# Performance work log

Hardware: AMD Instinct MI355X
Metric: run time of the kernel (lower is better)

## Reference

```python
import jax, jax.numpy as jnp
import numpy as np

B, S, N, T, F, E = 8, 4, 2000, 16, 10, 16
R = 8                      # rnn_hidden_unit
H1, H2 = 2 * R, R          # per-stock hidden sizes of lstm1 / lstm2
NH, DK, DV = 4, 8, 8       # attention heads / dims
DM = H2 * N                # attention model dim
D = R * T                  # node feature dim for hypergraph conv
MLP = 16
SLOPE = 0.1

def _layernorm(x, g, b, eps=1e-5):
    mu = x.mean(-1, keepdims=True)
    var = ((x - mu) ** 2).mean(-1, keepdims=True)
    return (x - mu) * jax.lax.rsqrt(var + eps) * g + b

def _lstm(x, W, U, b, h):
    # x: [B, N, T, e]; shared per-stock LSTM, scanned over time
    xt = jnp.moveaxis(x, 2, 0)                      # [T, B, N, e]
    z0 = jnp.zeros((x.shape[0], x.shape[1], h), x.dtype)
    def step(carry, xi):
        hp, cp = carry
        z = xi @ W + hp @ U + b                     # [B, N, 4h]
        i, f, g_, o = jnp.split(z, 4, axis=-1)
        c = jax.nn.sigmoid(f) * cp + jax.nn.sigmoid(i) * jnp.tanh(g_)
        hn = jax.nn.sigmoid(o) * jnp.tanh(c)
        return (hn, c), hn
    _, ys = jax.lax.scan(step, (z0, z0), xt)
    return jnp.moveaxis(ys, 0, 2)                   # [B, N, T, h]

def setup_inputs():
    key = jax.random.key(0)
    ks = jax.random.split(key, 24)
    g = lambda i, shape, s: jax.random.normal(ks[i], shape, dtype=jnp.float32) * s
    return {
        "inputs": jax.random.normal(ks[0], (B, N, T, F), dtype=jnp.float32),
        "emb_W": g(1, (F, E), 0.1), "emb_b": jnp.zeros((E,), jnp.float32),
        "W1": g(2, (E, 4 * H1), 0.1), "U1": g(3, (H1, 4 * H1), 0.1),
        "b1": jnp.zeros((4 * H1,), jnp.float32),
        "ln1_g": jnp.ones((N * H1,), jnp.float32), "ln1_b": jnp.zeros((N * H1,), jnp.float32),
        "W2": g(4, (H1, 4 * H2), 0.1), "U2": g(5, (H2, 4 * H2), 0.1),
        "b2": jnp.zeros((4 * H2,), jnp.float32),
        "Wq": g(6, (DM, NH * DK), 0.02), "Wk": g(7, (DM, NH * DK), 0.02),
        "Wv": g(8, (DM, NH * DV), 0.02), "Wo": g(9, (NH * DV, DM), 0.02),
        "ln2_g": jnp.ones((DM,), jnp.float32), "ln2_b": jnp.zeros((DM,), jnp.float32),
        "par": jax.random.uniform(ks[10], (S,), jnp.float32, 0.0, 0.99),
        "theta1": g(11, (D, D), 0.05), "diag1": jnp.ones((N,), jnp.float32),
        "theta2": g(12, (D, D), 0.05), "diag2": jnp.ones((N,), jnp.float32),
        "mlp1_W": g(13, (2 * R, MLP), 0.2), "mlp1_b": jnp.zeros((MLP,), jnp.float32),
        "mlp2_W": g(14, (MLP, 1), 0.2), "mlp2_b": jnp.zeros((1,), jnp.float32),
        "wavelets": g(15, (S, N, N), 0.02), "wavelets_inv": g(16, (S, N, N), 0.02),
    }

def reference(inputs, emb_W, emb_b, W1, U1, b1, ln1_g, ln1_b, W2, U2, b2,
              Wq, Wk, Wv, Wo, ln2_g, ln2_b, par, theta1, diag1, theta2, diag2,
              mlp1_W, mlp1_b, mlp2_W, mlp2_b, wavelets, wavelets_inv):
    x = inputs @ emb_W + emb_b                                  # [B,N,T,E]
    h1 = _lstm(x, W1, U1, b1, H1)                               # [B,N,T,H1]
    o = _layernorm(jnp.moveaxis(h1, 1, 2).reshape(B, T, N * H1), ln1_g, ln1_b)
    o = jnp.moveaxis(o.reshape(B, T, N, H1), 2, 1)              # [B,N,T,H1]
    h2 = _lstm(o, W2, U2, b2, H2)                               # [B,N,T,H2]
    enc = jnp.moveaxis(h2, 1, 2).reshape(B, T, DM)              # [B,T,DM]
    # causal multi-head temporal attention with residual + layernorm
    q = (enc @ Wq).reshape(B, T, NH, DK).transpose(0, 2, 1, 3)
    k = (enc @ Wk).reshape(B, T, NH, DK).transpose(0, 2, 1, 3)
    v = (enc @ Wv).reshape(B, T, NH, DV).transpose(0, 2, 1, 3)
    att = jnp.einsum('bhqd,bhkd->bhqk', q, k) / np.float32(np.sqrt(DK))
    causal = jnp.tril(jnp.ones((T, T), bool))
    att = jax.nn.softmax(jnp.where(causal, att, jnp.float32(-1e9)), axis=-1)
    ctx = jnp.einsum('bhqk,bhkd->bhqd', att, v).transpose(0, 2, 1, 3).reshape(B, T, NH * DV)
    enc = _layernorm(enc + ctx @ Wo, ln2_g, ln2_b)
    enc = enc.reshape(B, T, N, H2).transpose(0, 2, 1, 3)        # [B,N,T,H2]
    Xf = enc.reshape(B, N, D)                                   # per-sample node features
    # HWNN (approx=False): wavelets @ diag @ wavelets_inv @ (X @ theta), two layers,
    # vectorized over batch B and snapshots S (replaces the per-sample Python loop)
    X1 = jnp.einsum('bnd,de->bne', Xf, theta1)
    t1 = jnp.einsum('snm,bmd->bsnd', wavelets_inv, X1) * diag1[None, None, :, None]
    f1 = jax.nn.leaky_relu(jnp.einsum('snm,bsmd->bsnd', wavelets, t1), SLOPE)
    X2 = jnp.einsum('bsnd,de->bsne', f1, theta2)
    t2 = jnp.einsum('snm,bsmd->bsnd', wavelets_inv, X2) * diag2[None, None, :, None]
    f2 = jax.nn.leaky_relu(jnp.einsum('snm,bsmd->bsnd', wavelets, t2), SLOPE)
    hyper = jnp.einsum('s,bsnd->bnd', par, f2).reshape(B, N, T, H2)
    cat = jnp.concatenate([enc, hyper], axis=-1)                # [B,N,T,2R]
    m = jax.nn.relu(cat @ mlp1_W + mlp1_b)
    return (m @ mlp2_W + mlp2_b).reshape(B, N, T)
```

## Files before the change

kernel.cpp:

```cpp
#include <hip/hip_runtime.h>
#include <cstddef>

#define Bb 8
#define Ss 4
#define Nn 2000
#define Tt 16
#define Ee 16
#define H1 16
#define H2 8
#define DMm 16000

typedef __bf16 bf16;
typedef bf16 bf16x8 __attribute__((ext_vector_type(8)));
typedef float f32x4 __attribute__((ext_vector_type(4)));
#define GAS __attribute__((address_space(1)))
#define LAS __attribute__((address_space(3)))

__global__ __launch_bounds__(256) void embed_kernel(
    const float* __restrict__ in, const float* __restrict__ eW,
    const float* __restrict__ eb, float* __restrict__ x)
{
    int g = blockIdx.x * 256 + threadIdx.x;
    int e = g & 15;
    int row = g >> 4;
    const float* ip = in + (size_t)row * 10;
    float a = eb[e];
    #pragma unroll
    for (int f = 0; f < 10; ++f) a += ip[f] * eW[f * 16 + e];
    x[g] = a;
}

__global__ __launch_bounds__(256) void lstm1_kernel(
    const float* __restrict__ x, const float* __restrict__ W1,
    const float* __restrict__ U1, const float* __restrict__ b1,
    float* __restrict__ h1)
{
    int tid = threadIdx.x;
    int lane = tid & 63, wid = tid >> 6;
    int p = blockIdx.x * 4 + wid;
    float wcol[16], ucol[16];
    #pragma unroll
    for (int e = 0; e < 16; ++e) wcol[e] = W1[e * 64 + lane];
    #pragma unroll
    for (int k = 0; k < 16; ++k) ucol[k] = U1[k * 64 + lane];
    float bj = b1[lane];
    float hv = 0.f, cv = 0.f;
    const float* xp = x + (size_t)p * (Tt * Ee);
    float* hp = h1 + (size_t)p * (Tt * H1);
    for (int t = 0; t < Tt; ++t) {
        float xv = (lane < 16) ? xp[t * 16 + lane] : 0.f;
        float z = bj;
        #pragma unroll
        for (int e = 0; e < 16; ++e) z += __shfl(xv, e) * wcol[e];
        #pragma unroll
        for (int k = 0; k < 16; ++k) z += __shfl(hv, k) * ucol[k];
        float fz = __shfl(z, (lane + 16) & 63);
        float gz = __shfl(z, (lane + 32) & 63);
        float oz = __shfl(z, (lane + 48) & 63);
        if (lane < 16) {
            float ig = 1.f / (1.f + __expf(-z));
            float fg = 1.f / (1.f + __expf(-fz));
            float og = 1.f / (1.f + __expf(-oz));
            cv = fg * cv + ig * tanhf(gz);
            hv = og * tanhf(cv);
            hp[t * 16 + lane] = hv;
        }
    }
}

__global__ __launch_bounds__(256) void lstm2_kernel(
    const float* __restrict__ o1, const float* __restrict__ W2,
    const float* __restrict__ U2, const float* __restrict__ b2,
    float* __restrict__ h2)
{
    int tid = threadIdx.x;
    int lane = tid & 63, wid = tid >> 6;
    int j = lane & 31, half = lane >> 5, base = half << 5;
    int p = blockIdx.x * 8 + wid * 2 + half;
    float wcol[16], ucol[8];
    #pragma unroll
    for (int e = 0; e < 16; ++e) wcol[e] = W2[e * 32 + j];
    #pragma unroll
    for (int k = 0; k < 8; ++k) ucol[k] = U2[k * 32 + j];
    float bj = b2[j];
    float hv = 0.f, cv = 0.f;
    const float* op = o1 + (size_t)p * (Tt * H1);
    float* hp = h2 + (size_t)p * (Tt * H2);
    for (int t = 0; t < Tt; ++t) {
        float xv = (j < 16) ? op[t * 16 + j] : 0.f;
        float z = bj;
        #pragma unroll
        for (int e = 0; e < 16; ++e) z += __shfl(xv, base + e) * wcol[e];
        #pragma unroll
        for (int k = 0; k < 8; ++k) z += __shfl(hv, base + k) * ucol[k];
        float fz = __shfl(z, base + ((j + 8) & 31));
        float gz = __shfl(z, base + ((j + 16) & 31));
        float oz = __shfl(z, base + ((j + 24) & 31));
        if (j < 8) {
            float ig = 1.f / (1.f + __expf(-z));
            float fg = 1.f / (1.f + __expf(-fz));
            float og = 1.f / (1.f + __expf(-oz));
            cv = fg * cv + ig * tanhf(gz);
            hv = og * tanhf(cv);
            hp[t * 8 + j] = hv;
        }
    }
}

template<int NW>
__device__ __forceinline__ void block_reduce2t(float& a, float& b)
{
    #pragma unroll
    for (int off = 32; off; off >>= 1) {
        a += __shfl_xor(a, off);
        b += __shfl_xor(b, off);
    }
    __shared__ float r[2 * NW];
    int tid = threadIdx.x;
    if ((tid & 63) == 0) { r[tid >> 6] = a; r[NW + (tid >> 6)] = b; }
    __syncthreads();
    a = 0.f; b = 0.f;
    #pragma unroll
    for (int w = 0; w < NW; ++w) { a += r[w]; b += r[NW + w]; }
}

__global__ __launch_bounds__(1024) void ln1_kernel(
    const float* __restrict__ h1, const float* __restrict__ g,
    const float* __restrict__ bta, float* __restrict__ o1)
{
    int b = blockIdx.x >> 4, t = blockIdx.x & 15;
    int tid = threadIdx.x;
    float sum = 0.f, sq = 0.f;
    for (int i = tid; i < Nn * H1; i += 1024) {
        int n = i >> 4, j = i & 15;
        float v = h1[(((size_t)b * Nn + n) * Tt + t) * H1 + j];
        sum += v; sq += v * v;
    }
    block_reduce2t<16>(sum, sq);
    float mu = sum * (1.f / (Nn * H1));
    float var = sq * (1.f / (Nn * H1)) - mu * mu;
    float rstd = rsqrtf(var + 1e-5f);
    for (int i = tid; i < Nn * H1; i += 1024) {
        int n = i >> 4, j = i & 15;
        size_t idx = (((size_t)b * Nn + n) * Tt + t) * H1 + j;
        o1[idx] = (h1[idx] - mu) * rstd * g[i] + bta[i];
    }
}

__global__ __launch_bounds__(256) void transp_kernel(
    const float* __restrict__ h2, float* __restrict__ enc)
{
    int g = blockIdx.x * 256 + threadIdx.x;
    int r = g & 127;
    int p = g >> 7;
    int b = p / Nn, n = p % Nn;
    enc[(size_t)(b * 16 + (r >> 3)) * DMm + n * 8 + (r & 7)] = h2[g];
}

__global__ __launch_bounds__(192) void qkv_part_kernel(
    const float* __restrict__ enc, const float* __restrict__ Wq,
    const float* __restrict__ Wk, const float* __restrict__ Wv,
    float* __restrict__ partial)
{
    __shared__ float encT[500 * 16];
    int ks = blockIdx.x, btg = blockIdx.y;
    int tid = threadIdx.x;
    int k0 = ks * 500;
    for (int idx = tid; idx < 8000; idx += 192) {
        int kk = idx >> 4, r = idx & 15;
        encT[idx] = enc[(size_t)(btg * 16 + r) * DMm + k0 + kk];
    }
    __syncthreads();
    int c = tid % 96, rg = tid / 96;
    int cc = c & 31;
    const float* W = (c < 32) ? Wq : ((c < 64) ? Wk : Wv);
    float acc[8] = {};
    for (int kk = 0; kk < 500; ++kk) {
        float w = W[(size_t)(k0 + kk) * 32 + cc];
        const float* e = &encT[kk * 16 + rg * 8];
        #pragma unroll
        for (int r8 = 0; r8 < 8; ++r8) acc[r8] += e[r8] * w;
    }
    #pragma unroll
    for (int r8 = 0; r8 < 8; ++r8)
        partial[((size_t)ks * 128 + btg * 16 + rg * 8 + r8) * 96 + c] = acc[r8];
}

__global__ __launch_bounds__(256) void qkv_red_kernel(
    const float* __restrict__ partial, float* __restrict__ qb,
    float* __restrict__ kb, float* __restrict__ vb)
{
    int o = blockIdx.x * 256 + threadIdx.x;
    int bt = o / 96, c = o % 96;
    float v = 0.f;
    for (int ks = 0; ks < 32; ++ks) v += partial[(size_t)ks * 12288 + o];
    int b = bt >> 4, t = bt & 15;
    int cc = c & 31, h = cc >> 3, dk = cc & 7;
    float* dst = (c < 32) ? qb : ((c < 64) ? kb : vb);
    dst[(((size_t)b * 4 + h) * 16 + t) * 8 + dk] = v;
}

__global__ __launch_bounds__(256) void attn_kernel(
    const float* __restrict__ qb, const float* __restrict__ kb,
    const float* __restrict__ vb, float* __restrict__ ctx)
{
    int bh = blockIdx.x;
    int b = bh >> 2, h = bh & 3;
    __shared__ float qs[128], ks[128], vs[128], att[16][16];
    int tid = threadIdx.x;
    if (tid < 128) {
        qs[tid] = qb[(size_t)bh * 128 + tid];
        ks[tid] = kb[(size_t)bh * 128 + tid];
        vs[tid] = vb[(size_t)bh * 128 + tid];
    }
    __syncthreads();
    int qt = tid >> 4, kt = tid & 15;
    float s = -1e9f;
    if (kt <= qt) {
        float d = 0.f;
        #pragma unroll
        for (int x = 0; x < 8; ++x) d += qs[qt * 8 + x] * ks[kt * 8 + x];
        s = d * 0.35355339059327373f;
    }
    float mx = s;
    #pragma unroll
    for (int off = 8; off; off >>= 1) mx = fmaxf(mx, __shfl_xor(mx, off, 16));
    float p = __expf(s - mx);
    float sm = p;
    #pragma unroll
    for (int off = 8; off; off >>= 1) sm += __shfl_xor(sm, off, 16);
    att[qt][kt] = p / sm;
    __syncthreads();
    if (tid < 128) {
        int q2 = tid >> 3, dv = tid & 7;
        float cacc = 0.f;
        #pragma unroll
        for (int k2 = 0; k2 < 16; ++k2) cacc += att[q2][k2] * vs[k2 * 8 + dv];
        ctx[((size_t)b * 16 + q2) * 32 + h * 8 + dv] = cacc;
    }
}

__global__ __launch_bounds__(256) void ctxwo_kernel(
    const float* __restrict__ ctx, const float* __restrict__ Wo,
    float* __restrict__ resid2)
{
    int bt = blockIdx.y;
    int m = blockIdx.x * 256 + threadIdx.x;
    __shared__ float cs[32];
    if (threadIdx.x < 32) cs[threadIdx.x] = ctx[(size_t)bt * 32 + threadIdx.x];
    __syncthreads();
    if (m < DMm) {
        float acc = 0.f;
        #pragma unroll
        for (int j = 0; j < 32; ++j) acc += cs[j] * Wo[(size_t)j * DMm + m];
        resid2[(size_t)bt * DMm + m] = acc;
    }
}

__global__ __launch_bounds__(1024) void ln2_kernel(
    const float* __restrict__ enc, float* __restrict__ resid2,
    const float* __restrict__ g2, const float* __restrict__ b2v,
    float* __restrict__ Xf, bf16* __restrict__ Xfb)
{
    int bt = blockIdx.x;
    int b = bt >> 4, t = bt & 15;
    int tid = threadIdx.x;
    float sum = 0.f, sq = 0.f;
    for (int m = tid; m < DMm; m += 1024) {
        float v = enc[(size_t)bt * DMm + m] + resid2[(size_t)bt * DMm + m];
        resid2[(size_t)bt * DMm + m] = v;
        sum += v; sq += v * v;
    }
    block_reduce2t<16>(sum, sq);
    float mu = sum * (1.f / DMm);
    float var = sq * (1.f / DMm) - mu * mu;
    float rstd = rsqrtf(var + 1e-5f);
    for (int m = tid; m < DMm; m += 1024) {
        float v = resid2[(size_t)bt * DMm + m];
        float y = (v - mu) * rstd * g2[m] + b2v[m];
        int n = m >> 3, j = m & 7;
        size_t o = (size_t)n * 1024 + b * 128 + t * 8 + j;
        Xf[o] = y;
        Xfb[o] = (bf16)y;
    }
}

__global__ __launch_bounds__(256) void cvt_pad_kernel(
    const float* __restrict__ src, bf16* __restrict__ dst)
{
    int row = blockIdx.x;
    int tid = threadIdx.x;
    if (tid >= 252) return;
    int col = tid * 8;
    bf16 pk[8];
    if (col < 2000) {
        float4 v0 = *(const float4*)(src + (size_t)row * 2000 + col);
        float4 v1 = *(const float4*)(src + (size_t)row * 2000 + col + 4);
        pk[0] = (bf16)v0.x; pk[1] = (bf16)v0.y; pk[2] = (bf16)v0.z; pk[3] = (bf16)v0.w;
        pk[4] = (bf16)v1.x; pk[5] = (bf16)v1.y; pk[6] = (bf16)v1.z; pk[7] = (bf16)v1.w;
    } else {
        #pragma unroll
        for (int i = 0; i < 8; ++i) pk[i] = (bf16)0.f;
    }
    *(uint4*)(dst + (size_t)row * 2016 + col) = *(uint4*)pk;
}

__global__ __launch_bounds__(64) void zero_pad_kernel(
    bf16* __restrict__ X1b, bf16* __restrict__ Gb, bf16* __restrict__ X2b)
{
    int row = blockIdx.x;
    int tid = threadIdx.x;
    if (tid >= 48) return;
    bf16* p;
    if (row < 1024) p = X1b + (size_t)row * 2048;
    else if (row < 5120) p = Gb + (size_t)(row - 1024) * 2048;
    else p = X2b + (size_t)(row - 5120) * 2048;
    p[2000 + tid] = (bf16)0.f;
}

__global__ __launch_bounds__(256) void thcvt_kernel(
    const float* __restrict__ th1, const float* __restrict__ th2,
    bf16* __restrict__ th1T, bf16* __restrict__ th2T)
{
    int g = blockIdx.x * 256 + threadIdx.x;
    int d = g >> 7, d0 = g & 127;
    th1T[g] = (bf16)th1[(size_t)d0 * 128 + d];
    th2T[g] = (bf16)th2[(size_t)d0 * 128 + d];
}

__global__ __launch_bounds__(256) void theta_mfma(
    const bf16* __restrict__ Act, long sAct, const bf16* __restrict__ thT,
    bf16* __restrict__ Out, long sOut)
{
    __shared__ bf16 As2[128 * 128];
    __shared__ bf16 Bs2[128 * 128];
    const int tid = threadIdx.x;
    const int lane = tid & 63, wave = tid >> 6;
    const int m0 = blockIdx.x * 128, b = blockIdx.y, s = blockIdx.z;
    const bf16* Ab = Act + (size_t)s * sAct + (size_t)m0 * 1024 + b * 128;
    #pragma unroll
    for (int r = 0; r < 8; ++r) {
        int c = r * 256 + wave * 64 + lane;
        int row = c >> 4, col8 = (c & 15) * 8;
        __builtin_amdgcn_global_load_lds(
            (const GAS unsigned int*)(Ab + (size_t)row * 1024 + col8),
            (LAS unsigned int*)(As2 + c * 8), 16, 0, 0);
        __builtin_amdgcn_global_load_lds(
            (const GAS unsigned int*)(thT + (size_t)row * 128 + col8),
            (LAS unsigned int*)(Bs2 + c * 8), 16, 0, 0);
    }
    __syncthreads();
    const int wr = wave >> 1, wc = wave & 1;
    const int fm = lane & 15, quad = lane >> 4;
    f32x4 acc[4][4] = {};
    #pragma unroll
    for (int ks = 0; ks < 4; ++ks) {
        bf16x8 af[4], bfv[4];
        #pragma unroll
        for (int i = 0; i < 4; ++i)
            af[i] = *(const bf16x8*)(As2 + (wr * 64 + i * 16 + fm) * 128 + ks * 32 + quad * 8);
        #pragma unroll
        for (int j = 0; j < 4; ++j)
            bfv[j] = *(const bf16x8*)(Bs2 + (wc * 64 + j * 16 + fm) * 128 + ks * 32 + quad * 8);
        #pragma unroll
        for (int i = 0; i < 4; ++i)
            #pragma unroll
            for (int j = 0; j < 4; ++j)
                acc[i][j] = __builtin_amdgcn_mfma_f32_16x16x32_bf16(
                    af[i], bfv[j], acc[i][j], 0, 0, 0);
    }
    const int fm4 = quad * 4;
    #pragma unroll
    for (int i = 0; i < 4; ++i) {
        int m = m0 + wr * 64 + i * 16 + fm4;
        if (m >= 2000) continue;
        #pragma unroll
        for (int j = 0; j < 4; ++j) {
            int d = wc * 64 + j * 16 + fm;
            f32x4 v = acc[i][j];
            bf16 pk[4] = {(bf16)v[0], (bf16)v[1], (bf16)v[2], (bf16)v[3]};
            *(uint2*)(Out + (size_t)s * sOut + (size_t)(b * 128 + d) * 2048 + m) = *(uint2*)pk;
        }
    }
}

__global__ __launch_bounds__(256) void hgemm_bf16(
    const bf16* __restrict__ A, long sA,
    const bf16* __restrict__ Bt, long sB,
    bf16* __restrict__ C, long sC,
    const float* __restrict__ rowscale, int mode)
{
    __shared__ bf16 As[128 * 32];
    __shared__ bf16 Bs[128 * 32];
    const int tid = threadIdx.x;
    const int lane = tid & 63, wave = tid >> 6;
    const int m0 = blockIdx.x * 128, n0 = blockIdx.y * 128;
    const int s = blockIdx.z;
    const bf16* Abase = A + (size_t)s * sA;
    const bf16* Bbase = Bt + (size_t)s * sB;
    const int wr = wave >> 1, wc = wave & 1;
    const int fm = lane & 15, quad = lane >> 4;

    const int c0 = wave * 128 + lane, c1 = c0 + 64;
    int rA0 = m0 + (c0 >> 2); if (rA0 > 1999) rA0 = 1999;
    int rA1 = m0 + (c1 >> 2); if (rA1 > 1999) rA1 = 1999;
    const bf16* a0p = Abase + (size_t)rA0 * 2016 + (c0 & 3) * 8;
    const bf16* a1p = Abase + (size_t)rA1 * 2016 + (c1 & 3) * 8;
    const bf16* b0p = Bbase + (size_t)(n0 + (c0 >> 2)) * 2048 + (c0 & 3) * 8;
    const bf16* b1p = Bbase + (size_t)(n0 + (c1 >> 2)) * 2048 + (c1 & 3) * 8;
    bf16* as0 = As + c0 * 8; bf16* as1 = As + c1 * 8;
    bf16* bs0 = Bs + c0 * 8; bf16* bs1 = Bs + c1 * 8;

    f32x4 acc[4][4] = {};
    for (int kt = 0; kt < 63; ++kt) {
        const int k0 = kt * 32;
        __builtin_amdgcn_global_load_lds((const GAS unsigned int*)(a0p + k0),
                                         (LAS unsigned int*)as0, 16, 0, 0);
        __builtin_amdgcn_global_load_lds((const GAS unsigned int*)(a1p + k0),
                                         (LAS unsigned int*)as1, 16, 0, 0);
        __builtin_amdgcn_global_load_lds((const GAS unsigned int*)(b0p + k0),
                                         (LAS unsigned int*)bs0, 16, 0, 0);
        __builtin_amdgcn_global_load_lds((const GAS unsigned int*)(b1p + k0),
                                         (LAS unsigned int*)bs1, 16, 0, 0);
        __syncthreads();
        bf16x8 af[4], bfv[4];
        #pragma unroll
        for (int i = 0; i < 4; ++i)
            af[i] = *(const bf16x8*)(As + (wr * 64 + i * 16 + fm) * 32 + quad * 8);
        #pragma unroll
        for (int j = 0; j < 4; ++j)
            bfv[j] = *(const bf16x8*)(Bs + (wc * 64 + j * 16 + fm) * 32 + quad * 8);
        #pragma unroll
        for (int i = 0; i < 4; ++i)
            #pragma unroll
            for (int j = 0; j < 4; ++j)
                acc[i][j] = __builtin_amdgcn_mfma_f32_16x16x32_bf16(
                    af[i], bfv[j], acc[i][j], 0, 0, 0);
        __syncthreads();
    }

    const int fm4 = quad * 4;
    if (mode == 0) {
        #pragma unroll
        for (int i = 0; i < 4; ++i) {
            int m = m0 + wr * 64 + i * 16 + fm4;
            if (m >= 2000) continue;
            #pragma unroll
            for (int j = 0; j < 4; ++j) {
                int n = n0 + wc * 64 + j * 16 + fm;
                f32x4 v = acc[i][j];
                float4 rs = *(const float4*)(rowscale + m);
                v[0] *= rs.x; v[1] *= rs.y; v[2] *= rs.z; v[3] *= rs.w;
                bf16 pk[4] = {(bf16)v[0], (bf16)v[1], (bf16)v[2], (bf16)v[3]};
                *(uint2*)(C + (size_t)s * sC + (size_t)n * 2048 + m) = *(uint2*)pk;
            }
        }
    } else {
        #pragma unroll
        for (int i = 0; i < 4; ++i) {
            int mb_ = m0 + wr * 64 + i * 16 + fm4;
            #pragma unroll
            for (int j = 0; j < 4; ++j) {
                int n = n0 + wc * 64 + j * 16 + fm;
                #pragma unroll
                for (int r = 0; r < 4; ++r) {
                    int m = mb_ + r;
                    if (m < 2000) {
                        float x = acc[i][j][r];
                        x = x > 0.f ? x : 0.1f * x;
                        C[(size_t)s * sC + (size_t)m * 1024 + n] = (bf16)x;
                    }
                }
            }
        }
    }
}

__global__ __launch_bounds__(256) void mlp_kernel(
    const float* __restrict__ Xf, const bf16* __restrict__ F2,
    const float* __restrict__ par, const float* __restrict__ W1m,
    const float* __restrict__ b1m, const float* __restrict__ W2m,
    const float* __restrict__ b2m, float* __restrict__ out)
{
    __shared__ float w1s[256], b1s[16], w2s[16];
    int tid = threadIdx.x;
    w1s[tid] = W1m[tid];
    if (tid < 16) { b1s[tid] = b1m[tid]; w2s[tid] = W2m[tid]; }
    __syncthreads();
    int g = blockIdx.x * 256 + tid;
    int t = g & 15;
    int r = g >> 4;
    int b = r / Nn, n = r % Nn;
    size_t base = (size_t)n * 1024 + b * 128 + t * 8;
    float p0 = par[0], p1 = par[1], p2 = par[2], p3 = par[3];
    float c[16];
    #pragma unroll
    for (int j = 0; j < 8; ++j) {
        c[j] = Xf[base + j];
        c[8 + j] = p0 * (float)F2[base + j]
                 + p1 * (float)F2[2097152 + base + j]
                 + p2 * (float)F2[4194304 + base + j]
                 + p3 * (float)F2[6291456 + base + j];
    }
    float acc = b2m[0];
    #pragma unroll
    for (int hh = 0; hh < 16; ++hh) {
        float hs = b1s[hh];
        #pragma unroll
        for (int cc = 0; cc < 16; ++cc) hs += c[cc] * w1s[cc * 16 + hh];
        acc += fmaxf(hs, 0.f) * w2s[hh];
    }
    out[g] = acc;
}

extern "C" void kernel_launch(void* const* d_in, const int* in_sizes, int n_in,
                              void* d_out, int out_size, void* d_ws, size_t ws_size,
                              hipStream_t stream)
{
    const float* inputs = (const float*)d_in[0];
    const float* emb_W  = (const float*)d_in[1];
    const float* emb_b  = (const float*)d_in[2];
    const float* W1     = (const float*)d_in[3];
    const float* U1     = (const float*)d_in[4];
    const float* b1     = (const float*)d_in[5];
    const float* ln1_g  = (const float*)d_in[6];
    const float* ln1_b  = (const float*)d_in[7];
    const float* W2     = (const float*)d_in[8];
    const float* U2     = (const float*)d_in[9];
    const float* b2     = (const float*)d_in[10];
    const float* Wq     = (const float*)d_in[11];
    const float* Wk     = (const float*)d_in[12];
    const float* Wv     = (const float*)d_in[13];
    const float* Wo     = (const float*)d_in[14];
    const float* ln2_g  = (const float*)d_in[15];
    const float* ln2_b  = (const float*)d_in[16];
    const float* par    = (const float*)d_in[17];
    const float* theta1 = (const float*)d_in[18];
    const float* diag1  = (const float*)d_in[19];
    const float* theta2 = (const float*)d_in[20];
    const float* diag2  = (const float*)d_in[21];
    const float* mlp1_W = (const float*)d_in[22];
    const float* mlp1_b = (const float*)d_in[23];
    const float* mlp2_W = (const float*)d_in[24];
    const float* mlp2_b = (const float*)d_in[25];
    const float* wav    = (const float*)d_in[26];
    const float* winv   = (const float*)d_in[27];
    float* ws  = (float*)d_ws;
    float* out = (float*)d_out;

    float* xemb   = ws + 0;
    float* h1     = ws + 4096000;
    float* o1     = ws + 0;
    float* h2     = ws + 8192000;
    float* enc    = ws + 10240000;
    float* qpart  = ws + 12288000;
    float* qb     = ws + 12681216;
    float* kb     = ws + 12685312;
    float* vb     = ws + 12689408;
    float* ctx    = ws + 12693504;
    float* resid2 = ws + 4096000;
    float* Xf     = ws + 16128000;
    bf16*  Xfb    = (bf16*)(ws + 18176000);
    bf16*  wavb   = (bf16*)(ws + 0);
    bf16*  winvb  = (bf16*)(ws + 8064000);
    bf16*  X1b    = (bf16*)(ws + 19224576);
    bf16*  Gb     = (bf16*)(ws + 20273152);
    bf16*  Fb     = (bf16*)(ws + 24467456);
    bf16*  X2b    = (bf16*)(ws + 28661760);
    bf16*  F2b    = (bf16*)(ws + 24467456);
    bf16*  th1T   = (bf16*)(ws + 32856064);
    bf16*  th2T   = (bf16*)(ws + 32864256);

    embed_kernel<<<16000, 256, 0, stream>>>(inputs, emb_W, emb_b, xemb);
    lstm1_kernel<<<4000, 256, 0, stream>>>(xemb, W1, U1, b1, h1);
    ln1_kernel<<<128, 1024, 0, stream>>>(h1, ln1_g, ln1_b, o1);
    lstm2_kernel<<<2000, 256, 0, stream>>>(o1, W2, U2, b2, h2);
    transp_kernel<<<8000, 256, 0, stream>>>(h2, enc);
    qkv_part_kernel<<<dim3(32, 8), 192, 0, stream>>>(enc, Wq, Wk, Wv, qpart);
    qkv_red_kernel<<<48, 256, 0, stream>>>(qpart, qb, kb, vb);
    attn_kernel<<<32, 256, 0, stream>>>(qb, kb, vb, ctx);
    ctxwo_kernel<<<dim3(63, 128), 256, 0, stream>>>(ctx, Wo, resid2);
    ln2_kernel<<<128, 1024, 0, stream>>>(enc, resid2, ln2_g, ln2_b, Xf, Xfb);

    cvt_pad_kernel<<<8000, 256, 0, stream>>>(wav, wavb);
    cvt_pad_kernel<<<8000, 256, 0, stream>>>(winv, winvb);
    thcvt_kernel<<<64, 256, 0, stream>>>(theta1, theta2, th1T, th2T);
    zero_pad_kernel<<<9216, 64, 0, stream>>>(X1b, Gb, X2b);

    const long sW = 4032000;
    const long sAct = 2097152;
    theta_mfma<<<dim3(16, 8, 1), 256, 0, stream>>>(Xfb, 0, th1T, X1b, 0);
    hgemm_bf16<<<dim3(16, 8, 4), 256, 0, stream>>>(winvb, sW, X1b, 0, Gb, sAct, diag1, 0);
    hgemm_bf16<<<dim3(16, 8, 4), 256, 0, stream>>>(wavb, sW, Gb, sAct, Fb, sAct, nullptr, 1);
    theta_mfma<<<dim3(16, 8, 4), 256, 0, stream>>>(Fb, sAct, th2T, X2b, sAct);
    hgemm_bf16<<<dim3(16, 8, 4), 256, 0, stream>>>(winvb, sW, X2b, sAct, Gb, sAct, diag2, 0);
    hgemm_bf16<<<dim3(16, 8, 4), 256, 0, stream>>>(wavb, sW, Gb, sAct, F2b, sAct, nullptr, 1);

    mlp_kernel<<<1000, 256, 0, stream>>>(Xf, F2b, par, mlp1_W, mlp1_b,
                                         mlp2_W, mlp2_b, out);
}
```

Baseline: 731.6 us.

## Fold embedding into LSTM input weights, precompute gate inputs, remap LSTM lanes

The embedding matrix is folded into the first LSTM's input weights by a tiny setup kernel. The input-to-gate projections of both LSTMs are then precomputed in separate wide, parallel kernels. The recurrent kernels are remapped so each lane holds all four gates of one hidden unit. Hidden state is broadcast with ds_swizzle within 16-lane (or 8-lane) groups instead of full-wave shuffles, and tanh uses an exp-based formula. This cuts wasted lanes and shuffle latency in the sequential recurrence, at the cost of writing and re-reading larger precomputed gate tensors through global memory.

```diff
diff --git a/kernel.cpp b/kernel.cpp
--- a/kernel.cpp
+++ b/kernel.cpp
@@ -1,7 +1,6 @@
 #include <hip/hip_runtime.h>
 #include <cstddef>
 
-#define Bb 8
 #define Ss 4
 #define Nn 2000
 #define Tt 16
@@ -16,94 +15,135 @@
 #define GAS __attribute__((address_space(1)))
 #define LAS __attribute__((address_space(3)))
 
-__global__ __launch_bounds__(256) void embed_kernel(
-    const float* __restrict__ in, const float* __restrict__ eW,
-    const float* __restrict__ eb, float* __restrict__ x)
-{
-    int g = blockIdx.x * 256 + threadIdx.x;
-    int e = g & 15;
-    int row = g >> 4;
+__global__ __launch_bounds__(704) void wf_kernel(
+    const float* __restrict__ eW, const float* __restrict__ eb,
+    const float* __restrict__ W1, const float* __restrict__ b1,
+    float* __restrict__ Wf, float* __restrict__ bfv)
+{
+    int tid = threadIdx.x;
+    if (tid < 640) {
+        int f = tid >> 6, g = tid & 63;
+        float a = 0.f;
+        #pragma unroll
+        for (int e = 0; e < 16; ++e) a += eW[f * 16 + e] * W1[e * 64 + g];
+        Wf[f * 64 + g] = a;
+    } else if (tid < 704) {
+        int g = tid - 640;
+        float a = b1[g];
+        #pragma unroll
+        for (int e = 0; e < 16; ++e) a += eb[e] * W1[e * 64 + g];
+        bfv[g] = a;
+    }
+}
+
+__global__ __launch_bounds__(256) void zx1_kernel(
+    const float* __restrict__ in, const float* __restrict__ Wf,
+    const float* __restrict__ bfv, float* __restrict__ Zx)
+{
+    int gidx = blockIdx.x * 256 + threadIdx.x;
+    int g = gidx & 63;
+    int row = gidx >> 6;
     const float* ip = in + (size_t)row * 10;
-    float a = eb[e];
-    #pragma unroll
-    for (int f = 0; f < 10; ++f) a += ip[f] * eW[f * 16 + e];
-    x[g] = a;
-}
+    float a = bfv[g];
+    #pragma unroll
+    for (int f = 0; f < 10; ++f) a += ip[f] * Wf[f * 64 + g];
+    Zx[gidx] = a;
+}
+
+__global__ __launch_bounds__(256) void zx2_kernel(
+    const float* __restrict__ o1, const float* __restrict__ W2,
+    const float* __restrict__ b2, float* __restrict__ Zx2)
+{
+    int gidx = blockIdx.x * 256 + threadIdx.x;
+    int g = gidx & 31;
+    int row = gidx >> 5;
+    const float* op = o1 + (size_t)row * 16;
+    float a = b2[g];
+    #pragma unroll
+    for (int e = 0; e < 16; ++e) a += op[e] * W2[e * 32 + g];
+    Zx2[gidx] = a;
+}
+
+__device__ __forceinline__ float sigm(float x) { return 1.f / (1.f + __expf(-x)); }
+__device__ __forceinline__ float tanh_f(float x) { return 2.f / (1.f + __expf(-2.f * x)) - 1.f; }
 
 __global__ __launch_bounds__(256) void lstm1_kernel(
-    const float* __restrict__ x, const float* __restrict__ W1,
-    const float* __restrict__ U1, const float* __restrict__ b1,
+    const float* __restrict__ Zx, const float* __restrict__ U1,
     float* __restrict__ h1)
 {
     int tid = threadIdx.x;
     int lane = tid & 63, wid = tid >> 6;
-    int p = blockIdx.x * 4 + wid;
-    float wcol[16], ucol[16];
-    #pragma unroll
-    for (int e = 0; e < 16; ++e) wcol[e] = W1[e * 64 + lane];
-    #pragma unroll
-    for (int k = 0; k < 16; ++k) ucol[k] = U1[k * 64 + lane];
-    float bj = b1[lane];
+    int pl = lane >> 4, j = lane & 15;
+    int p = blockIdx.x * 16 + wid * 4 + pl;
+    float u[16][4];
+    #pragma unroll
+    for (int k = 0; k < 16; ++k)
+        #pragma unroll
+        for (int q = 0; q < 4; ++q)
+            u[k][q] = U1[k * 64 + q * 16 + j];
     float hv = 0.f, cv = 0.f;
-    const float* xp = x + (size_t)p * (Tt * Ee);
-    float* hp = h1 + (size_t)p * (Tt * H1);
-    for (int t = 0; t < Tt; ++t) {
-        float xv = (lane < 16) ? xp[t * 16 + lane] : 0.f;
-        float z = bj;
-        #pragma unroll
-        for (int e = 0; e < 16; ++e) z += __shfl(xv, e) * wcol[e];
-        #pragma unroll
-        for (int k = 0; k < 16; ++k) z += __shfl(hv, k) * ucol[k];
-        float fz = __shfl(z, (lane + 16) & 63);
-        float gz = __shfl(z, (lane + 32) & 63);
-        float oz = __shfl(z, (lane + 48) & 63);
-        if (lane < 16) {
-            float ig = 1.f / (1.f + __expf(-z));
-            float fg = 1.f / (1.f + __expf(-fz));
-            float og = 1.f / (1.f + __expf(-oz));
-            cv = fg * cv + ig * tanhf(gz);
-            hv = og * tanhf(cv);
-            hp[t * 16 + lane] = hv;
+    const float* zp = Zx + (size_t)p * (16 * 64);
+    float* hp = h1 + (size_t)p * (16 * 16);
+    for (int t = 0; t < 16; ++t) {
+        float zi = zp[t * 64 + j];
+        float zf = zp[t * 64 + 16 + j];
+        float zg = zp[t * 64 + 32 + j];
+        float zo = zp[t * 64 + 48 + j];
+        #define LSTM1_STEP(k)                                                        \
+        {                                                                            \
+            float hk = __int_as_float(__builtin_amdgcn_ds_swizzle(                   \
+                __float_as_int(hv), ((k) << 5) | 0x10));                             \
+            zi += hk * u[k][0]; zf += hk * u[k][1];                                  \
+            zg += hk * u[k][2]; zo += hk * u[k][3];                                  \
         }
+        LSTM1_STEP(0) LSTM1_STEP(1) LSTM1_STEP(2) LSTM1_STEP(3)
+        LSTM1_STEP(4) LSTM1_STEP(5) LSTM1_STEP(6) LSTM1_STEP(7)
+        LSTM1_STEP(8) LSTM1_STEP(9) LSTM1_STEP(10) LSTM1_STEP(11)
+        LSTM1_STEP(12) LSTM1_STEP(13) LSTM1_STEP(14) LSTM1_STEP(15)
+        #undef LSTM1_STEP
+        float ig = sigm(zi), fg = sigm(zf), og = sigm(zo);
+        cv = fg * cv + ig * tanh_f(zg);
+        hv = og * tanh_f(cv);
+        hp[t * 16 + j] = hv;
     }
 }
 
 __global__ __launch_bounds__(256) void lstm2_kernel(
-    const float* __restrict__ o1, const float* __restrict__ W2,
-    const float* __restrict__ U2, const float* __restrict__ b2,
+    const float* __restrict__ Zx2, const float* __restrict__ U2,
     float* __restrict__ h2)
 {
     int tid = threadIdx.x;
     int lane = tid & 63, wid = tid >> 6;
-    int j = lane & 31, half = lane >> 5, base = half << 5;
-    int p = blockIdx.x * 8 + wid * 2 + half;
-    float wcol[16], ucol[8];
-    #pragma unroll
-    for (int e = 0; e < 16; ++e) wcol[e] = W2[e * 32 + j];
-    #pragma unroll
-    for (int k = 0; k < 8; ++k) ucol[k] = U2[k * 32 + j];
-    float bj = b2[j];
+    int pg = lane >> 3, j = lane & 7;
+    int p = blockIdx.x * 32 + wid * 8 + pg;
+    float u[8][4];
+    #pragma unroll
+    for (int k = 0; k < 8; ++k)
+        #pragma unroll
+        for (int q = 0; q < 4; ++q)
+            u[k][q] = U2[k * 32 + q * 8 + j];
     float hv = 0.f, cv = 0.f;
-    const float* op = o1 + (size_t)p * (Tt * H1);
-    float* hp = h2 + (size_t)p * (Tt * H2);
-    for (int t = 0; t < Tt; ++t) {
-        float xv = (j < 16) ? op[t * 16 + j] : 0.f;
-        float z = bj;
-        #pragma unroll
-        for (int e = 0; e < 16; ++e) z += __shfl(xv, base + e) * wcol[e];
-        #pragma unroll
-        for (int k = 0; k < 8; ++k) z += __shfl(hv, base + k) * ucol[k];
-        float fz = __shfl(z, base + ((j + 8) & 31));
-        float gz = __shfl(z, base + ((j + 16) & 31));
-        float oz = __shfl(z, base + ((j + 24) & 31));
-        if (j < 8) {
-            float ig = 1.f / (1.f + __expf(-z));
-            float fg = 1.f / (1.f + __expf(-fz));
-            float og = 1.f / (1.f + __expf(-oz));
-            cv = fg * cv + ig * tanhf(gz);
-            hv = og * tanhf(cv);
-            hp[t * 8 + j] = hv;
+    const float* zp = Zx2 + (size_t)p * (16 * 32);
+    float* hp = h2 + (size_t)p * (16 * 8);
+    for (int t = 0; t < 16; ++t) {
+        float zi = zp[t * 32 + j];
+        float zf = zp[t * 32 + 8 + j];
+        float zg = zp[t * 32 + 16 + j];
+        float zo = zp[t * 32 + 24 + j];
+        #define LSTM2_STEP(k)                                                        \
+        {                                                                            \
+            float hk = __int_as_float(__builtin_amdgcn_ds_swizzle(                   \
+                __float_as_int(hv), ((k) << 5) | 0x18));                             \
+            zi += hk * u[k][0]; zf += hk * u[k][1];                                  \
+            zg += hk * u[k][2]; zo += hk * u[k][3];                                  \
         }
+        LSTM2_STEP(0) LSTM2_STEP(1) LSTM2_STEP(2) LSTM2_STEP(3)
+        LSTM2_STEP(4) LSTM2_STEP(5) LSTM2_STEP(6) LSTM2_STEP(7)
+        #undef LSTM2_STEP
+        float ig = sigm(zi), fg = sigm(zf), og = sigm(zo);
+        cv = fg * cv + ig * tanh_f(zg);
+        hv = og * tanh_f(cv);
+        hp[t * 8 + j] = hv;
     }
 }
 
@@ -548,10 +588,11 @@
     float* ws  = (float*)d_ws;
     float* out = (float*)d_out;
 
-    float* xemb   = ws + 0;
-    float* h1     = ws + 4096000;
+    float* Zx1    = ws + 0;
+    float* h1     = ws + 16384000;
     float* o1     = ws + 0;
-    float* h2     = ws + 8192000;
+    float* Zx2    = ws + 4096000;
+    float* h2     = ws + 12288000;
     float* enc    = ws + 10240000;
     float* qpart  = ws + 12288000;
     float* qb     = ws + 12681216;
@@ -570,11 +611,15 @@
     bf16*  F2b    = (bf16*)(ws + 24467456);
     bf16*  th1T   = (bf16*)(ws + 32856064);
     bf16*  th2T   = (bf16*)(ws + 32864256);
-
-    embed_kernel<<<16000, 256, 0, stream>>>(inputs, emb_W, emb_b, xemb);
-    lstm1_kernel<<<4000, 256, 0, stream>>>(xemb, W1, U1, b1, h1);
+    float* Wf     = ws + 20480000;
+    float* bfB    = ws + 20480640;
+
+    wf_kernel<<<1, 704, 0, stream>>>(emb_W, emb_b, W1, b1, Wf, bfB);
+    zx1_kernel<<<64000, 256, 0, stream>>>(inputs, Wf, bfB, Zx1);
+    lstm1_kernel<<<1000, 256, 0, stream>>>(Zx1, U1, h1);
     ln1_kernel<<<128, 1024, 0, stream>>>(h1, ln1_g, ln1_b, o1);
-    lstm2_kernel<<<2000, 256, 0, stream>>>(o1, W2, U2, b2, h2);
+    zx2_kernel<<<32000, 256, 0, stream>>>(o1, W2, b2, Zx2);
+    lstm2_kernel<<<500, 256, 0, stream>>>(Zx2, U2, h2);
     transp_kernel<<<8000, 256, 0, stream>>>(h2, enc);
     qkv_part_kernel<<<dim3(32, 8), 192, 0, stream>>>(enc, Wq, Wk, Wv, qpart);
     qkv_red_kernel<<<48, 256, 0, stream>>>(qpart, qb, kb, vb);
```

Result: faster. 701.5 us (-4.1%).
